# Kernel optimization log

Hardware: AMD Instinct MI355X
Metric: run time of the kernel (lower is better)

Reference implementation:

```python
import jax, jax.numpy as jnp
import numpy as np

DIM = 512
NUM_GROUPS = 32
NUM_HEADS = 8
EPS = 1e-5


def group_norm(x, gamma, beta):
    # x: (B, C, H, W); normalize over (C//G, H, W) per group
    B, C, H, W = x.shape
    g = x.reshape(B, NUM_GROUPS, -1)
    mean = g.mean(axis=2, keepdims=True)
    var = g.var(axis=2, keepdims=True)
    g = (g - mean) * jax.lax.rsqrt(var + EPS)
    x = g.reshape(B, C, H, W)
    return x * gamma[None, :, None, None] + beta[None, :, None, None]


def setup_inputs() -> dict:
    key = jax.random.key(0)
    ks = jax.random.split(key, 7)
    B, C, H, W = 16, DIM, 32, 32
    x = jax.random.normal(ks[0], (B, C, H, W), dtype=jnp.float32)
    gamma = jnp.ones((C,), dtype=jnp.float32)
    beta = jnp.zeros((C,), dtype=jnp.float32)
    s_in = 1.0 / np.sqrt(C)
    w_qkv = jax.random.normal(ks[1], (3 * C, C), dtype=jnp.float32) * s_in
    b_qkv = jnp.zeros((3 * C,), dtype=jnp.float32)
    w_proj = jax.random.normal(ks[2], (C, C), dtype=jnp.float32) * s_in
    b_proj = jnp.zeros((C,), dtype=jnp.float32)
    return {"x": x, "gamma": gamma, "beta": beta, "w_qkv": w_qkv,
            "b_qkv": b_qkv, "w_proj": w_proj, "b_proj": b_proj}


def reference(x, gamma, beta, w_qkv, b_qkv, w_proj, b_proj):
    B, C, H, W = x.shape
    nh = NUM_HEADS
    c3 = 3 * C // nh          # per-head qkv channels (3 * head_dim)
    dh = C // nh              # head_dim
    scale = C ** (-0.5)       # NOTE: source scales by full dim, not head_dim

    h = group_norm(x, gamma, beta)

    # 1x1 conv qkv projection: (B, 3C, H, W)
    qkv = jnp.einsum('bchw,oc->bohw', h, w_qkv) + b_qkv[None, :, None, None]

    # rearrange 'b (head c) h w -> (b head) (h w) c'
    qkv = qkv.reshape(B, nh, c3, H, W)
    qkv = qkv.transpose(0, 1, 3, 4, 2).reshape(B * nh, H * W, c3)
    q, k, v = jnp.split(qkv, 3, axis=2)   # each (B*nh, HW, dh)

    score = jnp.einsum('bnc,bmc->bnm', q, k * scale)   # (B*nh, HW, HW)
    attn = jax.nn.softmax(score, axis=2)
    out = jnp.einsum('bnm,bmc->bnc', attn, v)          # (B*nh, HW, dh)

    # rearrange '(head b) (h w) c -> b (head c) h w'  (NOTE head-major, as in source)
    out = out.reshape(nh, B, H, W, dh)
    out = out.transpose(1, 0, 4, 2, 3).reshape(B, C, H, W)

    out = jnp.einsum('bchw,oc->bohw', out, w_proj) + b_proj[None, :, None, None]
    return out + x
```

## Files before the change

kernel.cpp:

```cpp
#include <hip/hip_runtime.h>
#include <stdint.h>

typedef __bf16 bf16;
typedef __attribute__((ext_vector_type(4))) float f32x4;
typedef __attribute__((ext_vector_type(8))) __bf16 bf16x8;
typedef __attribute__((ext_vector_type(4))) __bf16 bf16x4;

#define NB 16
#define CH 512
#define HWS 1024
#define NHEAD 8
#define DH 64
#define O3 1536
#define LDP 72
#define CPQ 136
#define CPF 132

__global__ void prep(const float* __restrict__ x, float* __restrict__ stats,
                     const float* __restrict__ wq, const float* __restrict__ wp,
                     bf16* __restrict__ wq_b, bf16* __restrict__ wp_b) {
    int bx = blockIdx.x;
    if (bx < 512) {
        int b = bx >> 5, g = bx & 31;
        const float4* p = (const float4*)(x + ((size_t)(b * CH + g * 16)) * HWS);
        float s = 0.f, ss = 0.f;
        for (int i = threadIdx.x; i < 4096; i += 256) {
            float4 v = p[i];
            s  += v.x + v.y + v.z + v.w;
            ss += v.x*v.x + v.y*v.y + v.z*v.z + v.w*v.w;
        }
        for (int off = 32; off; off >>= 1) {
            s  += __shfl_xor(s,  off, 64);
            ss += __shfl_xor(ss, off, 64);
        }
        __shared__ float red[8];
        int w = threadIdx.x >> 6;
        if ((threadIdx.x & 63) == 0) { red[w*2] = s; red[w*2+1] = ss; }
        __syncthreads();
        if (threadIdx.x == 0) {
            float S  = red[0] + red[2] + red[4] + red[6];
            float SS = red[1] + red[3] + red[5] + red[7];
            float mean = S * (1.f/16384.f);
            float var  = SS * (1.f/16384.f) - mean*mean;
            stats[bx*2]   = mean;
            stats[bx*2+1] = rsqrtf(var + 1e-5f);
        }
    } else {
        int i = (bx - 512) * 256 + threadIdx.x;
        if (i < O3*CH) wq_b[i] = (bf16)wq[i];
        else           wp_b[i - O3*CH] = (bf16)wp[i - O3*CH];
    }
}

__global__ void gn_apply_t(const float* __restrict__ x, const float* __restrict__ stats,
                           const float* __restrict__ gamma, const float* __restrict__ beta,
                           bf16* __restrict__ hT) {
    __shared__ float tile[32][33];
    int bx = blockIdx.x;
    int b = bx >> 9;
    int rem = bx & 511;
    int ct = rem >> 5, nt = rem & 31;
    int tx = threadIdx.x & 31, ty = threadIdx.x >> 5;
    #pragma unroll
    for (int r = 0; r < 4; ++r) {
        int c = ct*32 + ty + r*8;
        int n = nt*32 + tx;
        float v = x[((size_t)(b * CH + c)) * HWS + n];
        int g = c >> 4;
        float mean = stats[(b*32+g)*2], rstd = stats[(b*32+g)*2+1];
        tile[ty + r*8][tx] = (v - mean) * rstd * gamma[c] + beta[c];
    }
    __syncthreads();
    #pragma unroll
    for (int r = 0; r < 4; ++r) {
        int n = nt*32 + ty + r*8;
        int c = ct*32 + tx;
        hT[((size_t)(b * HWS + n)) * CH + c] = (bf16)tile[tx][ty + r*8];
    }
}

__global__ __launch_bounds__(256, 3)
void qkv_gemm(const bf16* __restrict__ W, const bf16* __restrict__ hT,
              const float* __restrict__ bias, bf16* __restrict__ qkv,
              bf16* __restrict__ vT) {
    __shared__ __align__(16) bf16 SMEM[2*128*LDP];
    bf16* As = SMEM;
    bf16* Bs = SMEM + 128*LDP;
    int bx = blockIdx.x;
    int po = bx >> 7, qo = bx & 127;
    int obase = po*128, bnbase = qo*128;
    int tid = threadIdx.x;
    int lane = tid & 63, w = tid >> 6;
    int quad = lane >> 4, l15 = lane & 15;
    int wm = w >> 1, wn = w & 1;

    f32x4 acc[4][4] = {};
    for (int k0 = 0; k0 < 512; k0 += 64) {
        #pragma unroll
        for (int r = 0; r < 4; ++r) {
            int c = r*256 + tid;
            int row = c >> 3, dc = c & 7;
            uint4 va = *(const uint4*)(W  + ((size_t)(obase + row)) * 512 + k0 + dc*8);
            *(uint4*)(&As[row*LDP + dc*8]) = va;
            uint4 vb = *(const uint4*)(hT + ((size_t)(bnbase + row)) * 512 + k0 + dc*8);
            *(uint4*)(&Bs[row*LDP + dc*8]) = vb;
        }
        __syncthreads();
        #pragma unroll
        for (int ks = 0; ks < 2; ++ks) {
            bf16x8 af[4], bfv[4];
            #pragma unroll
            for (int mt = 0; mt < 4; ++mt)
                af[mt] = *(const bf16x8*)(&As[(wm*64 + mt*16 + l15)*LDP + ks*32 + quad*8]);
            #pragma unroll
            for (int nt = 0; nt < 4; ++nt)
                bfv[nt] = *(const bf16x8*)(&Bs[(wn*64 + nt*16 + l15)*LDP + ks*32 + quad*8]);
            #pragma unroll
            for (int mt = 0; mt < 4; ++mt)
                #pragma unroll
                for (int nt = 0; nt < 4; ++nt)
                    acc[mt][nt] = __builtin_amdgcn_mfma_f32_16x16x32_bf16(af[mt], bfv[nt], acc[mt][nt], 0, 0, 0);
        }
        __syncthreads();
    }

    bf16* Cs = SMEM;
    int b = bnbase >> 10;
    int nbase = bnbase & 1023;
    #pragma unroll
    for (int mt = 0; mt < 4; ++mt) {
        int o0 = obase + wm*64 + mt*16 + quad*4;
        float4 bb = *(const float4*)(bias + o0);
        int c192 = o0 % 192;
        bool isV = (c192 >= 128);
        int h = o0 / 192;
        int d0 = c192 - 128;
        #pragma unroll
        for (int nt = 0; nt < 4; ++nt) {
            int bn_l = wn*64 + nt*16 + l15;
            bf16x4 v;
            v[0] = (bf16)(acc[mt][nt][0] + bb.x);
            v[1] = (bf16)(acc[mt][nt][1] + bb.y);
            v[2] = (bf16)(acc[mt][nt][2] + bb.z);
            v[3] = (bf16)(acc[mt][nt][3] + bb.w);
            *(bf16x4*)(&Cs[bn_l*CPQ + (o0 - obase)]) = v;
            if (isV) {
                int key = nbase + bn_l;
                size_t vb_ = ((size_t)((b*8 + h)*64 + d0)) * HWS + key;
                vT[vb_]          = v[0];
                vT[vb_ + HWS]    = v[1];
                vT[vb_ + 2*HWS]  = v[2];
                vT[vb_ + 3*HWS]  = v[3];
            }
        }
    }
    __syncthreads();
    #pragma unroll
    for (int p = 0; p < 8; ++p) {
        int bn_l = p*16 + (tid >> 4);
        int o8 = (tid & 15) * 8;
        if ((obase + o8) % 192 < 128) {
            uint4 v = *(const uint4*)(&Cs[bn_l*CPQ + o8]);
            *(uint4*)(qkv + ((size_t)(bnbase + bn_l)) * O3 + obase + o8) = v;
        }
    }
}

__global__ __launch_bounds__(256, 4)
void flash_attn(const bf16* __restrict__ qkv, const bf16* __restrict__ vT,
                bf16* __restrict__ A2) {
    __shared__ __align__(16) bf16 Ks[64*LDP];
    __shared__ __align__(16) bf16 Vs[64*LDP];
    __shared__ __align__(16) bf16 Ps[4][32*LDP];
    int bx = blockIdx.x;
    int g = bx & 127, qt = bx >> 7;
    int b = g >> 3, h = g & 7;
    int tid = threadIdx.x, lane = tid & 63, w = tid >> 6;
    int quad = lane >> 4, l15 = lane & 15;
    const float kLog2 = 0.04419417382415922f * 1.44269504088896341f;

    bf16x8 aq[2][2];
    #pragma unroll
    for (int mt = 0; mt < 2; ++mt) {
        int qrow = qt*128 + w*32 + mt*16 + l15;
        const bf16* qb = qkv + ((size_t)(b * HWS + qrow)) * O3 + h*192;
        aq[mt][0] = *(const bf16x8*)(qb + quad*8);
        aq[mt][1] = *(const bf16x8*)(qb + 32 + quad*8);
    }

    f32x4 acc[2][4] = {};
    float L[2] = {0.f, 0.f};

    int r0 = tid >> 3, d0 = (tid & 7) * 8;
    int r1 = r0 + 32;
    const bf16* kp0 = qkv + ((size_t)(b * HWS + r0)) * O3 + h*192 + 64 + d0;
    const bf16* kp1 = qkv + ((size_t)(b * HWS + r1)) * O3 + h*192 + 64 + d0;
    const bf16* vp0 = vT + ((size_t)(g * DH + r0)) * HWS + d0;
    const bf16* vp1 = vT + ((size_t)(g * DH + r1)) * HWS + d0;
    bf16* ksd0 = &Ks[r0*LDP + d0];
    bf16* ksd1 = &Ks[r1*LDP + d0];
    bf16* vsd0 = &Vs[r0*LDP + d0];
    bf16* vsd1 = &Vs[r1*LDP + d0];

    uint4 ka = *(const uint4*)(kp0);
    uint4 kb = *(const uint4*)(kp1);
    uint4 va = *(const uint4*)(vp0);
    uint4 vb = *(const uint4*)(vp1);

    for (int kt = 0; kt < 16; ++kt) {
        __syncthreads();
        *(uint4*)ksd0 = ka;
        *(uint4*)ksd1 = kb;
        *(uint4*)vsd0 = va;
        *(uint4*)vsd1 = vb;
        __syncthreads();
        if (kt < 15) {
            size_t ko = (size_t)(kt+1) * 64 * O3;
            size_t vo = (size_t)(kt+1) * 64;
            ka = *(const uint4*)(kp0 + ko);
            kb = *(const uint4*)(kp1 + ko);
            va = *(const uint4*)(vp0 + vo);
            vb = *(const uint4*)(vp1 + vo);
        }

        #pragma unroll
        for (int nt = 0; nt < 4; ++nt) {
            bf16x8 ak0 = *(const bf16x8*)(&Ks[(nt*16 + l15)*LDP + quad*8]);
            bf16x8 ak1 = *(const bf16x8*)(&Ks[(nt*16 + l15)*LDP + 32 + quad*8]);
            #pragma unroll
            for (int mt = 0; mt < 2; ++mt) {
                f32x4 z = {};
                z = __builtin_amdgcn_mfma_f32_16x16x32_bf16(ak0, aq[mt][0], z, 0, 0, 0);
                z = __builtin_amdgcn_mfma_f32_16x16x32_bf16(ak1, aq[mt][1], z, 0, 0, 0);
                bf16x4 p;
                #pragma unroll
                for (int r = 0; r < 4; ++r) {
                    float e = exp2f(z[r] * kLog2);
                    L[mt] += e;
                    p[r] = (bf16)e;
                }
                *(bf16x4*)(&Ps[w][(mt*16 + l15)*LDP + nt*16 + quad*4]) = p;
            }
        }
        bf16x8 ap[2][2];
        #pragma unroll
        for (int mt = 0; mt < 2; ++mt) {
            ap[mt][0] = *(const bf16x8*)(&Ps[w][(mt*16 + l15)*LDP + quad*8]);
            ap[mt][1] = *(const bf16x8*)(&Ps[w][(mt*16 + l15)*LDP + 32 + quad*8]);
        }
        #pragma unroll
        for (int dt = 0; dt < 4; ++dt) {
            bf16x8 bv0 = *(const bf16x8*)(&Vs[(dt*16 + l15)*LDP + quad*8]);
            bf16x8 bv1 = *(const bf16x8*)(&Vs[(dt*16 + l15)*LDP + 32 + quad*8]);
            #pragma unroll
            for (int mt = 0; mt < 2; ++mt) {
                acc[mt][dt] = __builtin_amdgcn_mfma_f32_16x16x32_bf16(ap[mt][0], bv0, acc[mt][dt], 0, 0, 0);
                acc[mt][dt] = __builtin_amdgcn_mfma_f32_16x16x32_bf16(ap[mt][1], bv1, acc[mt][dt], 0, 0, 0);
            }
        }
    }

    float Linv[2][4];
    #pragma unroll
    for (int mt = 0; mt < 2; ++mt) {
        float Lf = L[mt];
        Lf += __shfl_xor(Lf, 16, 64);
        Lf += __shfl_xor(Lf, 32, 64);
        #pragma unroll
        for (int r = 0; r < 4; ++r)
            Linv[mt][r] = 1.f / __shfl(Lf, quad*4 + r, 64);
    }

    __syncthreads();
    #pragma unroll
    for (int mt = 0; mt < 2; ++mt)
        #pragma unroll
        for (int dt = 0; dt < 4; ++dt)
            #pragma unroll
            for (int r = 0; r < 4; ++r)
                Ps[w][(mt*16 + quad*4 + r)*LDP + dt*16 + l15] = (bf16)(acc[mt][dt][r] * Linv[mt][r]);

    int bp = g & 15;
    int hp = g >> 4;
    #pragma unroll
    for (int cc = 0; cc < 4; ++cc) {
        int c = cc*64 + lane;
        int row = c >> 3, dc = c & 7;
        uint4 v = *(const uint4*)(&Ps[w][row*LDP + dc*8]);
        size_t idx = ((size_t)(bp * HWS + qt*128 + w*32 + row)) * CH + hp*64 + dc*8;
        *(uint4*)(A2 + idx) = v;
    }
}

__global__ __launch_bounds__(256, 3)
void proj_gemm(const bf16* __restrict__ A2, const bf16* __restrict__ Wp,
               const float* __restrict__ bias, const float* __restrict__ x,
               float* __restrict__ out) {
    __shared__ __align__(16) bf16 SMEM[2*128*LDP];
    bf16* As = SMEM;
    bf16* Bs = SMEM + 128*LDP;
    int bx = blockIdx.x;
    int po = bx >> 7, qo = bx & 127;
    int obase = po*128, bnbase = qo*128;
    int tid = threadIdx.x;
    int lane = tid & 63, w = tid >> 6;
    int quad = lane >> 4, l15 = lane & 15;
    int wm = w >> 1, wn = w & 1;

    f32x4 acc[4][4] = {};
    for (int k0 = 0; k0 < 512; k0 += 64) {
        #pragma unroll
        for (int r = 0; r < 4; ++r) {
            int c = r*256 + tid;
            int row = c >> 3, dc = c & 7;
            uint4 va = *(const uint4*)(A2 + ((size_t)(bnbase + row)) * 512 + k0 + dc*8);
            *(uint4*)(&As[row*LDP + dc*8]) = va;
            uint4 vb = *(const uint4*)(Wp + ((size_t)(obase + row)) * 512 + k0 + dc*8);
            *(uint4*)(&Bs[row*LDP + dc*8]) = vb;
        }
        __syncthreads();
        #pragma unroll
        for (int ks = 0; ks < 2; ++ks) {
            bf16x8 af[4], bfv[4];
            #pragma unroll
            for (int mt = 0; mt < 4; ++mt)
                af[mt] = *(const bf16x8*)(&As[(wm*64 + mt*16 + l15)*LDP + ks*32 + quad*8]);
            #pragma unroll
            for (int nt = 0; nt < 4; ++nt)
                bfv[nt] = *(const bf16x8*)(&Bs[(wn*64 + nt*16 + l15)*LDP + ks*32 + quad*8]);
            #pragma unroll
            for (int mt = 0; mt < 4; ++mt)
                #pragma unroll
                for (int nt = 0; nt < 4; ++nt)
                    acc[mt][nt] = __builtin_amdgcn_mfma_f32_16x16x32_bf16(af[mt], bfv[nt], acc[mt][nt], 0, 0, 0);
        }
        __syncthreads();
    }

    float* Cf = (float*)SMEM;
    int bb = bnbase >> 10;
    int nbase = bnbase & 1023;
    #pragma unroll
    for (int hh = 0; hh < 2; ++hh) {
        if (wm == hh) {
            #pragma unroll
            for (int mt = 0; mt < 4; ++mt)
                #pragma unroll
                for (int nt = 0; nt < 4; ++nt)
                    #pragma unroll
                    for (int r = 0; r < 4; ++r)
                        Cf[(mt*16 + quad*4 + r)*CPF + wn*64 + nt*16 + l15] = acc[mt][nt][r];
        }
        __syncthreads();
        #pragma unroll
        for (int p = 0; p < 4; ++p) {
            int ol = p*32 + (tid >> 3);
            int nl0 = (tid & 7) * 8;
            int o = obase + ol;
            float bv = bias[o];
            #pragma unroll
            for (int jj = 0; jj < 2; ++jj) {
                int nl = nl0 + jj*4;
                size_t idx = ((size_t)(bb * CH + o)) * HWS + nbase + hh*64 + nl;
                float4 xr = *(const float4*)(x + idx);
                float4 res;
                res.x = Cf[(nl+0)*CPF + ol] + bv + xr.x;
                res.y = Cf[(nl+1)*CPF + ol] + bv + xr.y;
                res.z = Cf[(nl+2)*CPF + ol] + bv + xr.z;
                res.w = Cf[(nl+3)*CPF + ol] + bv + xr.w;
                *(float4*)(out + idx) = res;
            }
        }
        __syncthreads();
    }
}

extern "C" void kernel_launch(void* const* d_in, const int* in_sizes, int n_in,
                              void* d_out, int out_size, void* d_ws, size_t ws_size,
                              hipStream_t stream) {
    const float* x      = (const float*)d_in[0];
    const float* gamma  = (const float*)d_in[1];
    const float* beta   = (const float*)d_in[2];
    const float* w_qkv  = (const float*)d_in[3];
    const float* b_qkv  = (const float*)d_in[4];
    const float* w_proj = (const float*)d_in[5];
    const float* b_proj = (const float*)d_in[6];
    float* out = (float*)d_out;

    char* ws = (char*)d_ws;
    float* stats = (float*)(ws + 0);
    bf16*  wq_b  = (bf16*)(ws + 4096);
    bf16*  wp_b  = (bf16*)(ws + 1576960);
    bf16*  hT    = (bf16*)(ws + 2101248);
    bf16*  qkv   = (bf16*)(ws + 18878464);
    bf16*  vT    = (bf16*)(ws + 69210112);
    bf16*  A2    = hT;

    prep       <<<4608, 256, 0, stream>>>(x, stats, w_qkv, w_proj, wq_b, wp_b);
    gn_apply_t <<<8192, 256, 0, stream>>>(x, stats, gamma, beta, hT);
    qkv_gemm   <<<1536, 256, 0, stream>>>(wq_b, hT, b_qkv, qkv, vT);
    flash_attn <<<1024, 256, 0, stream>>>(qkv, vT, A2);
    proj_gemm  <<<512,  256, 0, stream>>>(A2, wp_b, b_proj, x, out);
}
```

Before: 220.2 us.

## Fuse groupnorm stats and apply, add register prefetch and XOR-swizzled LDS

Merges the groupnorm statistics and apply/transpose kernels into one kernel, so each block computes its group's stats and then normalizes and transposes the same group, re-reading x from cache instead of launching a second pass. Both GEMMs now prefetch the next K tile into registers while computing the current one, and store LDS tiles with an XOR swizzle instead of padding. Flash attention double-buffers its K/V LDS tiles, dropping one barrier per iteration, and lowers the occupancy hint from 4 to 3 blocks. The larger LDS and register footprint may reduce occupancy.

New measurement: 368.3 us. 1.67x slower.

```diff
diff --git a/kernel.cpp b/kernel.cpp
--- a/kernel.cpp
+++ b/kernel.cpp
@@ -12,70 +12,69 @@
 #define NHEAD 8
 #define DH 64
 #define O3 1536
+#define KLP 64
 #define LDP 72
 #define CPQ 136
 #define CPF 132
 
-__global__ void prep(const float* __restrict__ x, float* __restrict__ stats,
-                     const float* __restrict__ wq, const float* __restrict__ wp,
-                     bf16* __restrict__ wq_b, bf16* __restrict__ wp_b) {
+__global__ void gn_fused(const float* __restrict__ x,
+                         const float* __restrict__ gamma, const float* __restrict__ beta,
+                         const float* __restrict__ wq, const float* __restrict__ wp,
+                         bf16* __restrict__ wq_b, bf16* __restrict__ wp_b,
+                         bf16* __restrict__ hT) {
     int bx = blockIdx.x;
-    if (bx < 512) {
-        int b = bx >> 5, g = bx & 31;
-        const float4* p = (const float4*)(x + ((size_t)(b * CH + g * 16)) * HWS);
-        float s = 0.f, ss = 0.f;
-        for (int i = threadIdx.x; i < 4096; i += 256) {
-            float4 v = p[i];
-            s  += v.x + v.y + v.z + v.w;
-            ss += v.x*v.x + v.y*v.y + v.z*v.z + v.w*v.w;
-        }
-        for (int off = 32; off; off >>= 1) {
-            s  += __shfl_xor(s,  off, 64);
-            ss += __shfl_xor(ss, off, 64);
-        }
-        __shared__ float red[8];
-        int w = threadIdx.x >> 6;
-        if ((threadIdx.x & 63) == 0) { red[w*2] = s; red[w*2+1] = ss; }
-        __syncthreads();
-        if (threadIdx.x == 0) {
-            float S  = red[0] + red[2] + red[4] + red[6];
-            float SS = red[1] + red[3] + red[5] + red[7];
-            float mean = S * (1.f/16384.f);
-            float var  = SS * (1.f/16384.f) - mean*mean;
-            stats[bx*2]   = mean;
-            stats[bx*2+1] = rsqrtf(var + 1e-5f);
-        }
-    } else {
-        int i = (bx - 512) * 256 + threadIdx.x;
+    int tid = threadIdx.x;
+    if (bx >= 512) {
+        int i = (bx - 512) * 256 + tid;
         if (i < O3*CH) wq_b[i] = (bf16)wq[i];
         else           wp_b[i - O3*CH] = (bf16)wp[i - O3*CH];
-    }
-}
-
-__global__ void gn_apply_t(const float* __restrict__ x, const float* __restrict__ stats,
-                           const float* __restrict__ gamma, const float* __restrict__ beta,
-                           bf16* __restrict__ hT) {
-    __shared__ float tile[32][33];
-    int bx = blockIdx.x;
-    int b = bx >> 9;
-    int rem = bx & 511;
-    int ct = rem >> 5, nt = rem & 31;
-    int tx = threadIdx.x & 31, ty = threadIdx.x >> 5;
-    #pragma unroll
-    for (int r = 0; r < 4; ++r) {
-        int c = ct*32 + ty + r*8;
-        int n = nt*32 + tx;
-        float v = x[((size_t)(b * CH + c)) * HWS + n];
-        int g = c >> 4;
-        float mean = stats[(b*32+g)*2], rstd = stats[(b*32+g)*2+1];
-        tile[ty + r*8][tx] = (v - mean) * rstd * gamma[c] + beta[c];
-    }
+        return;
+    }
+    __shared__ float tile[16*68];
+    __shared__ float red[8];
+    __shared__ float sm[2];
+    int b = bx >> 5, g = bx & 31;
+    const float* xg = x + ((size_t)(b * CH + g * 16)) * HWS;
+    const float4* p4 = (const float4*)xg;
+    float s = 0.f, ss = 0.f;
+    for (int i = tid; i < 4096; i += 256) {
+        float4 v = p4[i];
+        s  += v.x + v.y + v.z + v.w;
+        ss += v.x*v.x + v.y*v.y + v.z*v.z + v.w*v.w;
+    }
+    for (int off = 32; off; off >>= 1) {
+        s  += __shfl_xor(s,  off, 64);
+        ss += __shfl_xor(ss, off, 64);
+    }
+    int w = tid >> 6;
+    if ((tid & 63) == 0) { red[w*2] = s; red[w*2+1] = ss; }
     __syncthreads();
-    #pragma unroll
-    for (int r = 0; r < 4; ++r) {
-        int n = nt*32 + ty + r*8;
-        int c = ct*32 + tx;
-        hT[((size_t)(b * HWS + n)) * CH + c] = (bf16)tile[tx][ty + r*8];
+    if (tid == 0) {
+        float S  = red[0] + red[2] + red[4] + red[6];
+        float SS = red[1] + red[3] + red[5] + red[7];
+        float mean = S * (1.f/16384.f);
+        float var  = SS * (1.f/16384.f) - mean*mean;
+        sm[0] = mean;
+        sm[1] = rsqrtf(var + 1e-5f);
+    }
+    __syncthreads();
+    float mean = sm[0], rstd = sm[1];
+    int cl = tid >> 4, nl4 = (tid & 15) * 4;
+    float sc = rstd * gamma[g*16 + cl];
+    float sh = beta[g*16 + cl] - mean * sc;
+    int nw = tid >> 2, c4 = tid & 3;
+    for (int nt = 0; nt < 16; ++nt) {
+        int n0 = nt * 64;
+        float4 v = *(const float4*)(xg + (size_t)cl * HWS + n0 + nl4);
+        float4 t;
+        t.x = v.x*sc + sh; t.y = v.y*sc + sh; t.z = v.z*sc + sh; t.w = v.w*sc + sh;
+        *(float4*)&tile[cl*68 + nl4] = t;
+        __syncthreads();
+        bf16x4 o;
+        #pragma unroll
+        for (int j = 0; j < 4; ++j) o[j] = (bf16)tile[(c4*4 + j)*68 + nw];
+        *(bf16x4*)(hT + ((size_t)(b * HWS + n0 + nw)) * CH + g*16 + c4*4) = o;
+        __syncthreads();
     }
 }
 
@@ -83,9 +82,9 @@
 void qkv_gemm(const bf16* __restrict__ W, const bf16* __restrict__ hT,
               const float* __restrict__ bias, bf16* __restrict__ qkv,
               bf16* __restrict__ vT) {
-    __shared__ __align__(16) bf16 SMEM[2*128*LDP];
+    __shared__ __align__(16) bf16 SMEM[128*CPQ];
     bf16* As = SMEM;
-    bf16* Bs = SMEM + 128*LDP;
+    bf16* Bs = SMEM + 128*KLP;
     int bx = blockIdx.x;
     int po = bx >> 7, qo = bx & 127;
     int obase = po*128, bnbase = qo*128;
@@ -93,28 +92,44 @@
     int lane = tid & 63, w = tid >> 6;
     int quad = lane >> 4, l15 = lane & 15;
     int wm = w >> 1, wn = w & 1;
+    int x7 = l15 & 7;
+
+    uint4 pa[4], pb[4];
+    #pragma unroll
+    for (int r = 0; r < 4; ++r) {
+        int c = r*256 + tid, row = c >> 3, dc = c & 7;
+        pa[r] = *(const uint4*)(W  + ((size_t)(obase + row)) * 512 + dc*8);
+        pb[r] = *(const uint4*)(hT + ((size_t)(bnbase + row)) * 512 + dc*8);
+    }
 
     f32x4 acc[4][4] = {};
     for (int k0 = 0; k0 < 512; k0 += 64) {
         #pragma unroll
         for (int r = 0; r < 4; ++r) {
-            int c = r*256 + tid;
-            int row = c >> 3, dc = c & 7;
-            uint4 va = *(const uint4*)(W  + ((size_t)(obase + row)) * 512 + k0 + dc*8);
-            *(uint4*)(&As[row*LDP + dc*8]) = va;
-            uint4 vb = *(const uint4*)(hT + ((size_t)(bnbase + row)) * 512 + k0 + dc*8);
-            *(uint4*)(&Bs[row*LDP + dc*8]) = vb;
-        }
-        __syncthreads();
+            int c = r*256 + tid, row = c >> 3, dc = c & 7;
+            int pc = row*KLP + ((dc ^ (row & 7)) * 8);
+            *(uint4*)(&As[pc]) = pa[r];
+            *(uint4*)(&Bs[pc]) = pb[r];
+        }
+        __syncthreads();
+        if (k0 < 448) {
+            #pragma unroll
+            for (int r = 0; r < 4; ++r) {
+                int c = r*256 + tid, row = c >> 3, dc = c & 7;
+                pa[r] = *(const uint4*)(W  + ((size_t)(obase + row)) * 512 + k0 + 64 + dc*8);
+                pb[r] = *(const uint4*)(hT + ((size_t)(bnbase + row)) * 512 + k0 + 64 + dc*8);
+            }
+        }
         #pragma unroll
         for (int ks = 0; ks < 2; ++ks) {
+            int ch = (ks*4 + quad) ^ x7;
             bf16x8 af[4], bfv[4];
             #pragma unroll
             for (int mt = 0; mt < 4; ++mt)
-                af[mt] = *(const bf16x8*)(&As[(wm*64 + mt*16 + l15)*LDP + ks*32 + quad*8]);
+                af[mt] = *(const bf16x8*)(&As[(wm*64 + mt*16 + l15)*KLP + ch*8]);
             #pragma unroll
             for (int nt = 0; nt < 4; ++nt)
-                bfv[nt] = *(const bf16x8*)(&Bs[(wn*64 + nt*16 + l15)*LDP + ks*32 + quad*8]);
+                bfv[nt] = *(const bf16x8*)(&Bs[(wn*64 + nt*16 + l15)*KLP + ch*8]);
             #pragma unroll
             for (int mt = 0; mt < 4; ++mt)
                 #pragma unroll
@@ -166,17 +181,18 @@
     }
 }
 
-__global__ __launch_bounds__(256, 4)
+__global__ __launch_bounds__(256, 3)
 void flash_attn(const bf16* __restrict__ qkv, const bf16* __restrict__ vT,
                 bf16* __restrict__ A2) {
-    __shared__ __align__(16) bf16 Ks[64*LDP];
-    __shared__ __align__(16) bf16 Vs[64*LDP];
+    __shared__ __align__(16) bf16 Kd[2][64*KLP];
+    __shared__ __align__(16) bf16 Vd[2][64*KLP];
     __shared__ __align__(16) bf16 Ps[4][32*LDP];
     int bx = blockIdx.x;
     int g = bx & 127, qt = bx >> 7;
     int b = g >> 3, h = g & 7;
     int tid = threadIdx.x, lane = tid & 63, w = tid >> 6;
     int quad = lane >> 4, l15 = lane & 15;
+    int x7 = l15 & 7;
     const float kLog2 = 0.04419417382415922f * 1.44269504088896341f;
 
     bf16x8 aq[2][2];
@@ -191,16 +207,14 @@
     f32x4 acc[2][4] = {};
     float L[2] = {0.f, 0.f};
 
-    int r0 = tid >> 3, d0 = (tid & 7) * 8;
+    int r0 = tid >> 3, dc = tid & 7, d0 = dc * 8;
     int r1 = r0 + 32;
+    int sOff0 = r0*KLP + ((dc ^ (r0 & 7)) * 8);
+    int sOff1 = r1*KLP + ((dc ^ (r0 & 7)) * 8);
     const bf16* kp0 = qkv + ((size_t)(b * HWS + r0)) * O3 + h*192 + 64 + d0;
     const bf16* kp1 = qkv + ((size_t)(b * HWS + r1)) * O3 + h*192 + 64 + d0;
     const bf16* vp0 = vT + ((size_t)(g * DH + r0)) * HWS + d0;
     const bf16* vp1 = vT + ((size_t)(g * DH + r1)) * HWS + d0;
-    bf16* ksd0 = &Ks[r0*LDP + d0];
-    bf16* ksd1 = &Ks[r1*LDP + d0];
-    bf16* vsd0 = &Vs[r0*LDP + d0];
-    bf16* vsd1 = &Vs[r1*LDP + d0];
 
     uint4 ka = *(const uint4*)(kp0);
     uint4 kb = *(const uint4*)(kp1);
@@ -208,11 +222,12 @@
     uint4 vb = *(const uint4*)(vp1);
 
     for (int kt = 0; kt < 16; ++kt) {
-        __syncthreads();
-        *(uint4*)ksd0 = ka;
-        *(uint4*)ksd1 = kb;
-        *(uint4*)vsd0 = va;
-        *(uint4*)vsd1 = vb;
+        bf16* Kb = &Kd[kt & 1][0];
+        bf16* Vb = &Vd[kt & 1][0];
+        *(uint4*)(Kb + sOff0) = ka;
+        *(uint4*)(Kb + sOff1) = kb;
+        *(uint4*)(Vb + sOff0) = va;
+        *(uint4*)(Vb + sOff1) = vb;
         __syncthreads();
         if (kt < 15) {
             size_t ko = (size_t)(kt+1) * 64 * O3;
@@ -225,8 +240,9 @@
 
         #pragma unroll
         for (int nt = 0; nt < 4; ++nt) {
-            bf16x8 ak0 = *(const bf16x8*)(&Ks[(nt*16 + l15)*LDP + quad*8]);
-            bf16x8 ak1 = *(const bf16x8*)(&Ks[(nt*16 + l15)*LDP + 32 + quad*8]);
+            int ro = (nt*16 + l15)*KLP;
+            bf16x8 ak0 = *(const bf16x8*)(&Kb[ro + ((quad ^ x7)*8)]);
+            bf16x8 ak1 = *(const bf16x8*)(&Kb[ro + (((4 + quad) ^ x7)*8)]);
             #pragma unroll
             for (int mt = 0; mt < 2; ++mt) {
                 f32x4 z = {};
@@ -250,8 +266,9 @@
         }
         #pragma unroll
         for (int dt = 0; dt < 4; ++dt) {
-            bf16x8 bv0 = *(const bf16x8*)(&Vs[(dt*16 + l15)*LDP + quad*8]);
-            bf16x8 bv1 = *(const bf16x8*)(&Vs[(dt*16 + l15)*LDP + 32 + quad*8]);
+            int ro = (dt*16 + l15)*KLP;
+            bf16x8 bv0 = *(const bf16x8*)(&Vb[ro + ((quad ^ x7)*8)]);
+            bf16x8 bv1 = *(const bf16x8*)(&Vb[ro + (((4 + quad) ^ x7)*8)]);
             #pragma unroll
             for (int mt = 0; mt < 2; ++mt) {
                 acc[mt][dt] = __builtin_amdgcn_mfma_f32_16x16x32_bf16(ap[mt][0], bv0, acc[mt][dt], 0, 0, 0);
@@ -285,9 +302,9 @@
     #pragma unroll
     for (int cc = 0; cc < 4; ++cc) {
         int c = cc*64 + lane;
-        int row = c >> 3, dc = c & 7;
-        uint4 v = *(const uint4*)(&Ps[w][row*LDP + dc*8]);
-        size_t idx = ((size_t)(bp * HWS + qt*128 + w*32 + row)) * CH + hp*64 + dc*8;
+        int row = c >> 3, dcc = c & 7;
+        uint4 v = *(const uint4*)(&Ps[w][row*LDP + dcc*8]);
+        size_t idx = ((size_t)(bp * HWS + qt*128 + w*32 + row)) * CH + hp*64 + dcc*8;
         *(uint4*)(A2 + idx) = v;
     }
 }
@@ -296,9 +313,9 @@
 void proj_gemm(const bf16* __restrict__ A2, const bf16* __restrict__ Wp,
                const float* __restrict__ bias, const float* __restrict__ x,
                float* __restrict__ out) {
-    __shared__ __align__(16) bf16 SMEM[2*128*LDP];
+    __shared__ __align__(16) bf16 SMEM[16896];
     bf16* As = SMEM;
-    bf16* Bs = SMEM + 128*LDP;
+    bf16* Bs = SMEM + 128*KLP;
     int bx = blockIdx.x;
     int po = bx >> 7, qo = bx & 127;
     int obase = po*128, bnbase = qo*128;
@@ -306,28 +323,44 @@
     int lane = tid & 63, w = tid >> 6;
     int quad = lane >> 4, l15 = lane & 15;
     int wm = w >> 1, wn = w & 1;
+    int x7 = l15 & 7;
+
+    uint4 pa[4], pb[4];
+    #pragma unroll
+    for (int r = 0; r < 4; ++r) {
+        int c = r*256 + tid, row = c >> 3, dc = c & 7;
+        pa[r] = *(const uint4*)(A2 + ((size_t)(bnbase + row)) * 512 + dc*8);
+        pb[r] = *(const uint4*)(Wp + ((size_t)(obase + row)) * 512 + dc*8);
+    }
 
     f32x4 acc[4][4] = {};
     for (int k0 = 0; k0 < 512; k0 += 64) {
         #pragma unroll
         for (int r = 0; r < 4; ++r) {
-            int c = r*256 + tid;
-            int row = c >> 3, dc = c & 7;
-            uint4 va = *(const uint4*)(A2 + ((size_t)(bnbase + row)) * 512 + k0 + dc*8);
-            *(uint4*)(&As[row*LDP + dc*8]) = va;
-            uint4 vb = *(const uint4*)(Wp + ((size_t)(obase + row)) * 512 + k0 + dc*8);
-            *(uint4*)(&Bs[row*LDP + dc*8]) = vb;
-        }
-        __syncthreads();
+            int c = r*256 + tid, row = c >> 3, dc = c & 7;
+            int pc = row*KLP + ((dc ^ (row & 7)) * 8);
+            *(uint4*)(&As[pc]) = pa[r];
+            *(uint4*)(&Bs[pc]) = pb[r];
+        }
+        __syncthreads();
+        if (k0 < 448) {
+            #pragma unroll
+            for (int r = 0; r < 4; ++r) {
+                int c = r*256 + tid, row = c >> 3, dc = c & 7;
+                pa[r] = *(const uint4*)(A2 + ((size_t)(bnbase + row)) * 512 + k0 + 64 + dc*8);
+                pb[r] = *(const uint4*)(Wp + ((size_t)(obase + row)) * 512 + k0 + 64 + dc*8);
+            }
+        }
         #pragma unroll
         for (int ks = 0; ks < 2; ++ks) {
+            int ch = (ks*4 + quad) ^ x7;
             bf16x8 af[4], bfv[4];
             #pragma unroll
             for (int mt = 0; mt < 4; ++mt)
-                af[mt] = *(const bf16x8*)(&As[(wm*64 + mt*16 + l15)*LDP + ks*32 + quad*8]);
+                af[mt] = *(const bf16x8*)(&As[(wm*64 + mt*16 + l15)*KLP + ch*8]);
             #pragma unroll
             for (int nt = 0; nt < 4; ++nt)
-                bfv[nt] = *(const bf16x8*)(&Bs[(wn*64 + nt*16 + l15)*LDP + ks*32 + quad*8]);
+                bfv[nt] = *(const bf16x8*)(&Bs[(wn*64 + nt*16 + l15)*KLP + ch*8]);
             #pragma unroll
             for (int mt = 0; mt < 4; ++mt)
                 #pragma unroll
@@ -388,7 +421,6 @@
     float* out = (float*)d_out;
 
     char* ws = (char*)d_ws;
-    float* stats = (float*)(ws + 0);
     bf16*  wq_b  = (bf16*)(ws + 4096);
     bf16*  wp_b  = (bf16*)(ws + 1576960);
     bf16*  hT    = (bf16*)(ws + 2101248);
@@ -396,9 +428,8 @@
     bf16*  vT    = (bf16*)(ws + 69210112);
     bf16*  A2    = hT;
 
-    prep       <<<4608, 256, 0, stream>>>(x, stats, w_qkv, w_proj, wq_b, wp_b);
-    gn_apply_t <<<8192, 256, 0, stream>>>(x, stats, gamma, beta, hT);
-    qkv_gemm   <<<1536, 256, 0, stream>>>(wq_b, hT, b_qkv, qkv, vT);
-    flash_attn <<<1024, 256, 0, stream>>>(qkv, vT, A2);
-    proj_gemm  <<<512,  256, 0, stream>>>(A2, wp_b, b_proj, x, out);
+    gn_fused  <<<4608, 256, 0, stream>>>(x, gamma, beta, w_qkv, w_proj, wq_b, wp_b, hT);
+    qkv_gemm  <<<1536, 256, 0, stream>>>(wq_b, hT, b_qkv, qkv, vT);
+    flash_attn<<<1024, 256, 0, stream>>>(qkv, vT, A2);
+    proj_gemm <<<512,  256, 0, stream>>>(A2, wp_b, b_proj, x, out);
 }
```
